# Kernel tuning notes

Hardware: AMD Instinct MI355X
Metric: run time of the kernel (lower is better)

The kernel has to match this reference:

```python
import jax, jax.numpy as jnp
import numpy as np

HID = 256


def _mlp(h, ws, bs):
    # 4-layer MLP: tanh x3, sigmoid output (matches nn.Sequential in torch code)
    h = jnp.tanh(h @ ws[0] + bs[0])
    h = jnp.tanh(h @ ws[1] + bs[1])
    h = jnp.tanh(h @ ws[2] + bs[2])
    return jax.nn.sigmoid(h @ ws[3] + bs[3])


def setup_inputs() -> dict:
    key = jax.random.key(0)
    N, K, DE = 100000, 32, 8
    IN1 = K * DE          # 256
    MID = 5
    IN2 = K * MID         # 160
    E = N * K
    ks = jax.random.split(key, 20)
    x = jax.random.normal(ks[0], (N, DE), dtype=jnp.float32)
    edge_index = jax.random.randint(ks[1], (2, E), 0, N, dtype=jnp.int64)
    edge_attr = jax.random.normal(ks[2], (E, DE), dtype=jnp.float32)

    def lin(k, fan_in, fan_out):
        kw, kb = jax.random.split(k)
        lim = 1.0 / np.sqrt(fan_in)
        w = jax.random.uniform(kw, (fan_in, fan_out), jnp.float32, -lim, lim)
        b = jax.random.uniform(kb, (fan_out,), jnp.float32, -lim, lim)
        return w, b

    dims1 = [(IN1, HID), (HID, HID), (HID, HID), (HID, MID)]
    dims2 = [(IN2, HID), (HID, HID), (HID, HID), (HID, 1)]
    inp = {"x": x, "edge_index": edge_index, "edge_attr": edge_attr}
    for i, (fi, fo) in enumerate(dims1):
        w, b = lin(ks[3 + i], fi, fo)
        inp[f"w1_{i}"], inp[f"b1_{i}"] = w, b
    for i, (fi, fo) in enumerate(dims2):
        w, b = lin(ks[10 + i], fi, fo)
        inp[f"w2_{i}"], inp[f"b2_{i}"] = w, b
    return inp


def reference(x, edge_index, edge_attr,
              w1_0, b1_0, w1_1, b1_1, w1_2, b1_2, w1_3, b1_3,
              w2_0, b2_0, w2_1, b2_1, w2_2, b2_2, w2_3, b2_3):
    K = 32
    IN1 = w1_0.shape[0]              # 256
    MID = w1_3.shape[1]              # 5
    # GNN1: message = edge_attr; aggregate reshapes to [N, IN1] then MLP -> [N, MID]
    out1 = _mlp(edge_attr.reshape(-1, IN1), (w1_0, w1_1, w1_2, w1_3), (b1_0, b1_1, b1_2, b1_3))
    # GNN2: message = x_j = out1[edge_index[1]] (flow='target_to_source')
    gathered = out1[edge_index[1]]                     # [E, MID] irregular gather
    out2 = _mlp(gathered.reshape(-1, K * MID), (w2_0, w2_1, w2_2, w2_3), (b2_0, b2_1, b2_2, b2_3))
    return out2[:, 0]                                  # squeeze dim 1 -> [N]
```

## Files before the change

kernel.cpp:

```cpp
#include <hip/hip_runtime.h>
#include <stdint.h>

typedef uint16_t u16;
typedef uint32_t u32;
typedef __attribute__((ext_vector_type(8)))  __bf16 bf16x8;
typedef __attribute__((ext_vector_type(16))) float  f32x16;
typedef __attribute__((ext_vector_type(4)))  float  f32x4;
typedef __attribute__((ext_vector_type(2)))  u32    u32x2;

#define NROWS   100000
#define E_EDGES 3200000

#define HIDX(r, g) (((r) << 8) + ((((g) ^ ((r) & 31))) << 3))

#define MFMA(a, b, c) __builtin_amdgcn_mfma_f32_32x32x16_bf16((a), (b), (c), 0, 0, 0)

__device__ __forceinline__ u32 bfpack(float a, float b) {
    u16 lo = __builtin_bit_cast(u16, (__bf16)a);
    u16 hi = __builtin_bit_cast(u16, (__bf16)b);
    return (u32)lo | ((u32)hi << 16);
}
__device__ __forceinline__ float fast_tanh(float x) {
    float e = __builtin_amdgcn_exp2f(x * 2.885390081777927f);
    float r = __builtin_amdgcn_rcpf(e + 1.0f);
    return __builtin_fmaf(-2.0f, r, 1.0f);
}
__device__ __forceinline__ float fast_sigmoid(float x) {
    float e = __builtin_amdgcn_exp2f(x * -1.4426950408889634f);
    return __builtin_amdgcn_rcpf(1.0f + e);
}

__device__ __forceinline__ void dense256(u16* __restrict__ Hs, const u16* __restrict__ WB,
                                         const float* __restrict__ bias,
                                         int wave, int l31, int lh) {
    f32x16 acc[4];
#pragma unroll
    for (int i = 0; i < 4; ++i)
#pragma unroll
        for (int j = 0; j < 16; ++j) acc[i][j] = 0.0f;

    const u16* wp = WB + (wave * 64 + l31) * 16 + lh * 8;
    bf16x8 wq0[3], wq1[3];
#pragma unroll
    for (int d = 0; d < 3; ++d) {
        wq0[d] = *(const bf16x8*)(wp + d * 4096);
        wq1[d] = *(const bf16x8*)(wp + d * 4096 + 512);
    }

    __syncthreads();

    bf16x8 hq0[2], hq1[2];
#pragma unroll
    for (int d = 0; d < 2; ++d) {
        const int g = 2 * d + lh;
        hq0[d] = *(const bf16x8*)(Hs + HIDX(l31, g));
        hq1[d] = *(const bf16x8*)(Hs + HIDX(32 + l31, g));
    }

#pragma unroll
    for (int s = 0; s < 16; ++s) {
        const int cw = s % 3, ch = s & 1;
        bf16x8 w0 = wq0[cw], w1 = wq1[cw], h0 = hq0[ch], h1 = hq1[ch];
        if (s + 3 < 16) {
            wq0[cw] = *(const bf16x8*)(wp + (s + 3) * 4096);
            wq1[cw] = *(const bf16x8*)(wp + (s + 3) * 4096 + 512);
        }
        if (s + 2 < 16) {
            const int ng = 2 * (s + 2) + lh;
            hq0[ch] = *(const bf16x8*)(Hs + HIDX(l31, ng));
            hq1[ch] = *(const bf16x8*)(Hs + HIDX(32 + l31, ng));
        }
        acc[0] = MFMA(w0, h0, acc[0]);
        acc[1] = MFMA(w0, h1, acc[1]);
        acc[2] = MFMA(w1, h0, acc[2]);
        acc[3] = MFMA(w1, h1, acc[3]);
    }
    __syncthreads();

#pragma unroll
    for (int i = 0; i < 2; ++i) {
        const int nt = wave * 2 + i;
#pragma unroll
        for (int rg = 0; rg < 4; ++rg) {
            const float4 bv = *(const float4*)(bias + nt * 32 + rg * 8 + lh * 4);
#pragma unroll
            for (int b = 0; b < 2; ++b) {
                const f32x16& A = acc[i * 2 + b];
                float x0 = fast_tanh(A[rg * 4 + 0] + bv.x);
                float x1 = fast_tanh(A[rg * 4 + 1] + bv.y);
                float x2 = fast_tanh(A[rg * 4 + 2] + bv.z);
                float x3 = fast_tanh(A[rg * 4 + 3] + bv.w);
                const int r = b * 32 + l31;
                const int g = nt * 4 + rg;
                uint2 v; v.x = bfpack(x0, x1); v.y = bfpack(x2, x3);
                *(uint2*)(Hs + (r << 8) + (((g) ^ (r & 31)) << 3) + lh * 4) = v;
            }
        }
    }
}

__device__ __forceinline__ f32x16 final_dense(const u16* __restrict__ Hs,
                                              const u16* __restrict__ WBf,
                                              int wave, int l31, int lh) {
    __syncthreads();
    f32x16 acc;
#pragma unroll
    for (int j = 0; j < 16; ++j) acc[j] = 0.0f;
    if (wave < 2) {
        const u16* wp = WBf + l31 * 16 + lh * 8;
        bf16x8 wq[2], hq[2];
#pragma unroll
        for (int d = 0; d < 2; ++d) {
            wq[d] = *(const bf16x8*)(wp + d * 512);
            hq[d] = *(const bf16x8*)(Hs + HIDX(wave * 32 + l31, 2 * d + lh));
        }
#pragma unroll
        for (int s = 0; s < 16; ++s) {
            const int c = s & 1;
            bf16x8 w = wq[c], h = hq[c];
            if (s + 2 < 16) {
                wq[c] = *(const bf16x8*)(wp + (s + 2) * 512);
                hq[c] = *(const bf16x8*)(Hs + HIDX(wave * 32 + l31, 2 * (s + 2) + lh));
            }
            acc = MFMA(w, h, acc);
        }
    }
    return acc;
}

__global__ __launch_bounds__(256, 4) void mlp1_kernel(
    const float* __restrict__ ea, const u16* __restrict__ WB1, const u16* __restrict__ WB13,
    const float* __restrict__ b0, const float* __restrict__ b1, const float* __restrict__ b2,
    const float* __restrict__ b3, u16* __restrict__ out1) {
    __shared__ u16 Hs[64 * 256];
    const int tid = threadIdx.x, wave = tid >> 6, lane = tid & 63, blk = blockIdx.x;
    const int l31 = lane & 31, lh = lane >> 5;

#pragma unroll
    for (int i = 0; i < 8; ++i) {
        const int li = i * 256 + tid;
        const int r = li >> 5, g = li & 31;
        const int rg_ = blk * 64 + r;
        uint4 v = {0u, 0u, 0u, 0u};
        if (rg_ < NROWS) {
            const float* p = ea + (size_t)rg_ * 256 + g * 8;
            f32x4 a0 = __builtin_nontemporal_load((const f32x4*)p);
            f32x4 a1 = __builtin_nontemporal_load((const f32x4*)p + 1);
            v.x = bfpack(a0.x, a0.y); v.y = bfpack(a0.z, a0.w);
            v.z = bfpack(a1.x, a1.y); v.w = bfpack(a1.z, a1.w);
        }
        *(uint4*)(Hs + HIDX(r, g)) = v;
    }
    dense256(Hs, WB1,          b0, wave, l31, lh);
    dense256(Hs, WB1 + 65536,  b1, wave, l31, lh);
    dense256(Hs, WB1 + 131072, b2, wave, l31, lh);
    f32x16 acc = final_dense(Hs, WB13, wave, l31, lh);

    if (wave < 2) {
        const int row_g = blk * 64 + wave * 32 + l31;
        if (row_g < NROWS) {
            if (lh == 0) {
                float s0 = fast_sigmoid(acc[0] + b3[0]);
                float s1 = fast_sigmoid(acc[1] + b3[1]);
                float s2 = fast_sigmoid(acc[2] + b3[2]);
                float s3 = fast_sigmoid(acc[3] + b3[3]);
                u32x2 v; v.x = bfpack(s0, s1); v.y = bfpack(s2, s3);
                __builtin_nontemporal_store(v, (u32x2*)(out1 + (size_t)row_g * 8));
            } else {
                float s4 = fast_sigmoid(acc[0] + b3[4]);
                u32x2 v; v.x = bfpack(s4, 0.0f); v.y = 0u;
                __builtin_nontemporal_store(v, (u32x2*)(out1 + (size_t)row_g * 8 + 4));
            }
        }
    }
}

__global__ __launch_bounds__(256, 4) void mlp2_kernel(
    const int* __restrict__ idx1, const u16* __restrict__ out1,
    const u16* __restrict__ WB2, const u16* __restrict__ WB23,
    const float* __restrict__ b0, const float* __restrict__ b1, const float* __restrict__ b2,
    const float* __restrict__ b3, float* __restrict__ out) {
    __shared__ u16 Hs[64 * 256];
    const int tid = threadIdx.x, wave = tid >> 6, lane = tid & 63, blk = blockIdx.x;
    const int l31 = lane & 31, lh = lane >> 5;

    int nodes[8];
#pragma unroll
    for (int i = 0; i < 8; ++i) {
        const long e = (long)blk * 2048 + i * 256 + tid;
        nodes[i] = (e < (long)E_EDGES) ? __builtin_nontemporal_load(idx1 + e) : -1;
    }
#pragma unroll
    for (int i = 0; i < 8; ++i) {
        const int li = i * 256 + tid;
        const int r = li >> 5, j = li & 31;
        uint4 v = {0u, 0u, 0u, 0u};
        if (nodes[i] >= 0) v = *(const uint4*)(out1 + (size_t)nodes[i] * 8);
        *(uint4*)(Hs + HIDX(r, j)) = v;
    }
    dense256(Hs, WB2,          b0, wave, l31, lh);
    dense256(Hs, WB2 + 65536,  b1, wave, l31, lh);
    dense256(Hs, WB2 + 131072, b2, wave, l31, lh);
    f32x16 acc = final_dense(Hs, WB23, wave, l31, lh);

    if (wave < 2) {
        const int row_g = blk * 64 + wave * 32 + l31;
        if (row_g < NROWS && lh == 0)
            __builtin_nontemporal_store(fast_sigmoid(acc[0] + b3[0]), out + row_g);
    }
}

__global__ void transform_kernel(
    const float* __restrict__ w10, const float* __restrict__ w11, const float* __restrict__ w12,
    const float* __restrict__ w13, const float* __restrict__ w20, const float* __restrict__ w21,
    const float* __restrict__ w22, const float* __restrict__ w23, u16* __restrict__ ws) {
    const int id = blockIdx.x * 256 + threadIdx.x;
    float val;
    if (id < 196608) {
        int layer = id >> 16, rem = id & 65535;
        int s = rem >> 12, n = (rem >> 4) & 255, kl = rem & 15;
        int k = s * 16 + kl;
        const float* w = layer == 0 ? w10 : (layer == 1 ? w11 : w12);
        val = w[k * 256 + n];
    } else if (id < 204800) {
        int rem = id - 196608;
        int s = rem >> 9, n = (rem >> 4) & 31, kl = rem & 15;
        int k = s * 16 + kl;
        val = (n < 5) ? w13[k * 5 + n] : 0.0f;
    } else if (id < 401408) {
        int rem = id - 204800;
        int layer = rem >> 16; rem &= 65535;
        int s = rem >> 12, n = (rem >> 4) & 255, kl = rem & 15;
        int k = s * 16 + kl;
        if (layer == 0) {
            int j = k >> 3, v = k & 7;
            val = (v < 5) ? w20[(j * 5 + v) * 256 + n] : 0.0f;
        } else {
            val = (layer == 1 ? w21 : w22)[k * 256 + n];
        }
    } else {
        int rem = id - 401408;
        int s = rem >> 9, n = (rem >> 4) & 31, kl = rem & 15;
        int k = s * 16 + kl;
        val = (n == 0) ? w23[k] : 0.0f;
    }
    u32 u = __builtin_bit_cast(u32, val);
    u = (u + 0x7FFFu + ((u >> 16) & 1u)) >> 16;
    ws[id] = (u16)u;
}

extern "C" void kernel_launch(void* const* d_in, const int* in_sizes, int n_in,
                              void* d_out, int out_size, void* d_ws, size_t ws_size,
                              hipStream_t stream) {
    const int*   ei  = (const int*)d_in[1];
    const float* ea  = (const float*)d_in[2];
    const float* w10 = (const float*)d_in[3];  const float* b10 = (const float*)d_in[4];
    const float* w11 = (const float*)d_in[5];  const float* b11 = (const float*)d_in[6];
    const float* w12 = (const float*)d_in[7];  const float* b12 = (const float*)d_in[8];
    const float* w13 = (const float*)d_in[9];  const float* b13 = (const float*)d_in[10];
    const float* w20 = (const float*)d_in[11]; const float* b20 = (const float*)d_in[12];
    const float* w21 = (const float*)d_in[13]; const float* b21 = (const float*)d_in[14];
    const float* w22 = (const float*)d_in[15]; const float* b22 = (const float*)d_in[16];
    const float* w23 = (const float*)d_in[17]; const float* b23 = (const float*)d_in[18];

    u16* ws   = (u16*)d_ws;
    u16* WB1  = ws;
    u16* WB13 = ws + 196608;
    u16* WB2  = ws + 204800;
    u16* WB23 = ws + 401408;
    u16* out1 = ws + 409600;

    hipLaunchKernelGGL(transform_kernel, dim3(1600), dim3(256), 0, stream,
                       w10, w11, w12, w13, w20, w21, w22, w23, ws);
    hipLaunchKernelGGL(mlp1_kernel, dim3(1563), dim3(256), 0, stream,
                       ea, WB1, WB13, b10, b11, b12, b13, out1);
    hipLaunchKernelGGL(mlp2_kernel, dim3(1563), dim3(256), 0, stream,
                       ei + E_EDGES, out1, WB2, WB23, b20, b21, b22, b23, (float*)d_out);
}
```

Measured before the change: 320.8 us.

## Process 128 rows per block with 512 threads and raise MFMA priority

Blocks double from 64 to 128 rows and from 4 to 8 waves. Each pair of wave groups shares the same weight column slice but works on different 64-row halves, so per-row launch and sync overhead is spread over more rows. It also wraps the MFMA issue in s_setprio so matrix work is prioritized over other waves' loads. Each block now needs 64KB of LDS and 512 threads, which may limit how many blocks fit per CU and lengthens the barriers.

```diff
diff --git a/kernel.cpp b/kernel.cpp
--- a/kernel.cpp
+++ b/kernel.cpp
@@ -10,6 +10,8 @@
 
 #define NROWS   100000
 #define E_EDGES 3200000
+#define ROWS_PB 128
+#define NBLK    782
 
 #define HIDX(r, g) (((r) << 8) + ((((g) ^ ((r) & 31))) << 3))
 
@@ -32,14 +34,14 @@
 
 __device__ __forceinline__ void dense256(u16* __restrict__ Hs, const u16* __restrict__ WB,
                                          const float* __restrict__ bias,
-                                         int wave, int l31, int lh) {
+                                         int nw, int rb, int l31, int lh) {
     f32x16 acc[4];
 #pragma unroll
     for (int i = 0; i < 4; ++i)
 #pragma unroll
         for (int j = 0; j < 16; ++j) acc[i][j] = 0.0f;
 
-    const u16* wp = WB + (wave * 64 + l31) * 16 + lh * 8;
+    const u16* wp = WB + (nw * 64 + l31) * 16 + lh * 8;
     bf16x8 wq0[3], wq1[3];
 #pragma unroll
     for (int d = 0; d < 3; ++d) {
@@ -53,8 +55,8 @@
 #pragma unroll
     for (int d = 0; d < 2; ++d) {
         const int g = 2 * d + lh;
-        hq0[d] = *(const bf16x8*)(Hs + HIDX(l31, g));
-        hq1[d] = *(const bf16x8*)(Hs + HIDX(32 + l31, g));
+        hq0[d] = *(const bf16x8*)(Hs + HIDX(rb + l31, g));
+        hq1[d] = *(const bf16x8*)(Hs + HIDX(rb + 32 + l31, g));
     }
 
 #pragma unroll
@@ -67,19 +69,21 @@
         }
         if (s + 2 < 16) {
             const int ng = 2 * (s + 2) + lh;
-            hq0[ch] = *(const bf16x8*)(Hs + HIDX(l31, ng));
-            hq1[ch] = *(const bf16x8*)(Hs + HIDX(32 + l31, ng));
-        }
+            hq0[ch] = *(const bf16x8*)(Hs + HIDX(rb + l31, ng));
+            hq1[ch] = *(const bf16x8*)(Hs + HIDX(rb + 32 + l31, ng));
+        }
+        __builtin_amdgcn_s_setprio(1);
         acc[0] = MFMA(w0, h0, acc[0]);
         acc[1] = MFMA(w0, h1, acc[1]);
         acc[2] = MFMA(w1, h0, acc[2]);
         acc[3] = MFMA(w1, h1, acc[3]);
+        __builtin_amdgcn_s_setprio(0);
     }
     __syncthreads();
 
 #pragma unroll
     for (int i = 0; i < 2; ++i) {
-        const int nt = wave * 2 + i;
+        const int nt = nw * 2 + i;
 #pragma unroll
         for (int rg = 0; rg < 4; ++rg) {
             const float4 bv = *(const float4*)(bias + nt * 32 + rg * 8 + lh * 4);
@@ -90,7 +94,7 @@
                 float x1 = fast_tanh(A[rg * 4 + 1] + bv.y);
                 float x2 = fast_tanh(A[rg * 4 + 2] + bv.z);
                 float x3 = fast_tanh(A[rg * 4 + 3] + bv.w);
-                const int r = b * 32 + l31;
+                const int r = rb + b * 32 + l31;
                 const int g = nt * 4 + rg;
                 uint2 v; v.x = bfpack(x0, x1); v.y = bfpack(x2, x3);
                 *(uint2*)(Hs + (r << 8) + (((g) ^ (r & 31)) << 3) + lh * 4) = v;
@@ -106,7 +110,7 @@
     f32x16 acc;
 #pragma unroll
     for (int j = 0; j < 16; ++j) acc[j] = 0.0f;
-    if (wave < 2) {
+    if (wave < 4) {
         const u16* wp = WBf + l31 * 16 + lh * 8;
         bf16x8 wq[2], hq[2];
 #pragma unroll
@@ -128,19 +132,20 @@
     return acc;
 }
 
-__global__ __launch_bounds__(256, 4) void mlp1_kernel(
+__global__ __launch_bounds__(512, 4) void mlp1_kernel(
     const float* __restrict__ ea, const u16* __restrict__ WB1, const u16* __restrict__ WB13,
     const float* __restrict__ b0, const float* __restrict__ b1, const float* __restrict__ b2,
     const float* __restrict__ b3, u16* __restrict__ out1) {
-    __shared__ u16 Hs[64 * 256];
+    __shared__ u16 Hs[ROWS_PB * 256];
     const int tid = threadIdx.x, wave = tid >> 6, lane = tid & 63, blk = blockIdx.x;
     const int l31 = lane & 31, lh = lane >> 5;
+    const int nw = wave & 3, rb = (wave >> 2) * 64;
 
 #pragma unroll
     for (int i = 0; i < 8; ++i) {
-        const int li = i * 256 + tid;
+        const int li = i * 512 + tid;
         const int r = li >> 5, g = li & 31;
-        const int rg_ = blk * 64 + r;
+        const int rg_ = blk * ROWS_PB + r;
         uint4 v = {0u, 0u, 0u, 0u};
         if (rg_ < NROWS) {
             const float* p = ea + (size_t)rg_ * 256 + g * 8;
@@ -151,13 +156,13 @@
         }
         *(uint4*)(Hs + HIDX(r, g)) = v;
     }
-    dense256(Hs, WB1,          b0, wave, l31, lh);
-    dense256(Hs, WB1 + 65536,  b1, wave, l31, lh);
-    dense256(Hs, WB1 + 131072, b2, wave, l31, lh);
+    dense256(Hs, WB1,          b0, nw, rb, l31, lh);
+    dense256(Hs, WB1 + 65536,  b1, nw, rb, l31, lh);
+    dense256(Hs, WB1 + 131072, b2, nw, rb, l31, lh);
     f32x16 acc = final_dense(Hs, WB13, wave, l31, lh);
 
-    if (wave < 2) {
-        const int row_g = blk * 64 + wave * 32 + l31;
+    if (wave < 4) {
+        const int row_g = blk * ROWS_PB + wave * 32 + l31;
         if (row_g < NROWS) {
             if (lh == 0) {
                 float s0 = fast_sigmoid(acc[0] + b3[0]);
@@ -175,36 +180,37 @@
     }
 }
 
-__global__ __launch_bounds__(256, 4) void mlp2_kernel(
+__global__ __launch_bounds__(512, 4) void mlp2_kernel(
     const int* __restrict__ idx1, const u16* __restrict__ out1,
     const u16* __restrict__ WB2, const u16* __restrict__ WB23,
     const float* __restrict__ b0, const float* __restrict__ b1, const float* __restrict__ b2,
     const float* __restrict__ b3, float* __restrict__ out) {
-    __shared__ u16 Hs[64 * 256];
+    __shared__ u16 Hs[ROWS_PB * 256];
     const int tid = threadIdx.x, wave = tid >> 6, lane = tid & 63, blk = blockIdx.x;
     const int l31 = lane & 31, lh = lane >> 5;
+    const int nw = wave & 3, rb = (wave >> 2) * 64;
 
     int nodes[8];
 #pragma unroll
     for (int i = 0; i < 8; ++i) {
-        const long e = (long)blk * 2048 + i * 256 + tid;
+        const long e = (long)blk * 4096 + i * 512 + tid;
         nodes[i] = (e < (long)E_EDGES) ? __builtin_nontemporal_load(idx1 + e) : -1;
     }
 #pragma unroll
     for (int i = 0; i < 8; ++i) {
-        const int li = i * 256 + tid;
+        const int li = i * 512 + tid;
         const int r = li >> 5, j = li & 31;
         uint4 v = {0u, 0u, 0u, 0u};
         if (nodes[i] >= 0) v = *(const uint4*)(out1 + (size_t)nodes[i] * 8);
         *(uint4*)(Hs + HIDX(r, j)) = v;
     }
-    dense256(Hs, WB2,          b0, wave, l31, lh);
-    dense256(Hs, WB2 + 65536,  b1, wave, l31, lh);
-    dense256(Hs, WB2 + 131072, b2, wave, l31, lh);
+    dense256(Hs, WB2,          b0, nw, rb, l31, lh);
+    dense256(Hs, WB2 + 65536,  b1, nw, rb, l31, lh);
+    dense256(Hs, WB2 + 131072, b2, nw, rb, l31, lh);
     f32x16 acc = final_dense(Hs, WB23, wave, l31, lh);
 
-    if (wave < 2) {
-        const int row_g = blk * 64 + wave * 32 + l31;
+    if (wave < 4) {
+        const int row_g = blk * ROWS_PB + wave * 32 + l31;
         if (row_g < NROWS && lh == 0)
             __builtin_nontemporal_store(fast_sigmoid(acc[0] + b3[0]), out + row_g);
     }
@@ -272,8 +278,8 @@
 
     hipLaunchKernelGGL(transform_kernel, dim3(1600), dim3(256), 0, stream,
                        w10, w11, w12, w13, w20, w21, w22, w23, ws);
-    hipLaunchKernelGGL(mlp1_kernel, dim3(1563), dim3(256), 0, stream,
+    hipLaunchKernelGGL(mlp1_kernel, dim3(NBLK), dim3(512), 0, stream,
                        ea, WB1, WB13, b10, b11, b12, b13, out1);
-    hipLaunchKernelGGL(mlp2_kernel, dim3(1563), dim3(256), 0, stream,
+    hipLaunchKernelGGL(mlp2_kernel, dim3(NBLK), dim3(512), 0, stream,
                        ei + E_EDGES, out1, WB2, WB23, b20, b21, b22, b23, (float*)d_out);
 }
```

Measured after the change: 437.0 us. 1.36x slower.
